# Optimization experiments

Measured on AMD Instinct MI355X. Metric: run time of the kernel, lower is better.

Reference implementation:

```python
import jax, jax.numpy as jnp
import numpy as np

B, LC, LQ, D = 32, 2048, 256, 256


def setup_inputs() -> dict:
    key = jax.random.key(0)
    kc, kq, kcm, kqm, kw = jax.random.split(key, 5)
    context = jax.random.normal(kc, (B, LC, D), dtype=jnp.float32)
    query = jax.random.normal(kq, (B, LQ, D), dtype=jnp.float32)
    # True = masked (matches torch masked_fill semantics)
    context_mask = jax.random.randint(kcm, (B, LC), 0, 2).astype(bool)
    query_mask = jax.random.randint(kqm, (B, LQ), 0, 2).astype(bool)
    # nn.Linear(3*dim, 1, bias=False) weight, flattened to (3D,)
    w0 = jax.random.normal(kw, (3 * D,), dtype=jnp.float32) * (1.0 / np.sqrt(3 * D))
    return {"context": context, "query": query, "context_mask": context_mask,
            "query_mask": query_mask, "w0": w0}


def reference(context, query, context_mask, query_mask, w0):
    d = context.shape[-1]
    wc, wq, wm = w0[:d], w0[d:2 * d], w0[2 * d:]
    # trilinear sim: w0 . [c, q, c*q]  ==  c.wc + q.wq + (c*wm) q^T
    sc = context @ wc                                   # (B, Lc)
    sq = query @ wq                                     # (B, Lq)
    sim = sc[:, :, None] + sq[:, None, :] + jnp.einsum(
        'bcd,bqd->bcq', context * wm, query)            # (B, Lc, Lq)
    mask = context_mask[:, :, None] | query_mask[:, None, :]
    sim = jnp.where(mask, jnp.float32(-1e30), sim)
    S = jax.nn.softmax(sim, axis=-1)                    # row softmax over Lq
    SS = jax.nn.softmax(sim, axis=1)                    # col softmax over Lc
    S = jnp.nan_to_num(S)
    SS = jnp.nan_to_num(SS)
    A = jnp.einsum('bcq,bqd->bcd', S, query)            # (B, Lc, D)
    T = jnp.einsum('bkq,bkd->bqd', SS, context)         # SS^T @ context, (B, Lq, D)
    Bmat = jnp.einsum('bcq,bqd->bcd', S, T)             # (B, Lc, D)
    return (A, Bmat)
```

## Files before the change

kernel.cpp:

```cpp
#include <hip/hip_runtime.h>

#define B_  32
#define LC_ 2048
#define LQ_ 256
#define D_  256
#define NEG (-1e30f)

typedef _Float16 f16;
typedef _Float16 f16x4 __attribute__((ext_vector_type(4)));
typedef _Float16 f16x8 __attribute__((ext_vector_type(8)));
typedef float    f32x4 __attribute__((ext_vector_type(4)));

__global__ __launch_bounds__(256) void k_scsq(
    const float* __restrict__ ctx, const float* __restrict__ qry,
    const float* __restrict__ w0, float* __restrict__ sc, float* __restrict__ sq)
{
    const int lane = threadIdx.x & 63;
    const int wave = threadIdx.x >> 6;
    const int row  = blockIdx.x * 4 + wave;
    const int NC = B_ * LC_;
    const int NQ = B_ * LQ_;
    const float* src; const float* w; float* dst;
    if (row < NC) { src = ctx + (long long)row * D_; w = w0; dst = sc + row; }
    else if (row < NC + NQ) { int r = row - NC; src = qry + (long long)r * D_; w = w0 + D_; dst = sq + r; }
    else return;
    float4 a = *(const float4*)(src + lane * 4);
    float4 b = *(const float4*)(w   + lane * 4);
    float v = a.x*b.x + a.y*b.y + a.z*b.z + a.w*b.w;
    #pragma unroll
    for (int off = 32; off > 0; off >>= 1) v += __shfl_down(v, off, 64);
    if (lane == 0) *dst = v;
}

__global__ __launch_bounds__(256) void k_transpose_q(
    const float* __restrict__ in, f16* __restrict__ out,
    int R, int C, long long in_bs, long long out_bs)
{
    __shared__ float tile[64 * 65];
    const int b = blockIdx.z;
    const int r0 = blockIdx.x * 64, c0 = blockIdx.y * 64;
    const int t = threadIdx.x;
    const float* ib = in + (long long)b * in_bs;
    #pragma unroll
    for (int p = 0; p < 4; ++p) {
        int r = (t >> 4) + p * 16;
        int cb = (t & 15) * 4;
        float4 v = *(const float4*)(ib + (long long)(r0 + r) * C + c0 + cb);
        tile[r * 65 + cb + 0] = v.x;
        tile[r * 65 + cb + 1] = v.y;
        tile[r * 65 + cb + 2] = v.z;
        tile[r * 65 + cb + 3] = v.w;
    }
    __syncthreads();
    f16* ob = out + (long long)b * out_bs;
    #pragma unroll
    for (int p = 0; p < 4; ++p) {
        int c = (t >> 4) + p * 16;
        int rb = (t & 15) * 4;
        f16x4 h;
        h[0] = (f16)tile[(rb + 0) * 65 + c];
        h[1] = (f16)tile[(rb + 1) * 65 + c];
        h[2] = (f16)tile[(rb + 2) * 65 + c];
        h[3] = (f16)tile[(rb + 3) * 65 + c];
        *(f16x4*)(ob + (long long)(c0 + c) * R + r0 + rb) = h;
    }
}

#define LDA1 40
__global__ __launch_bounds__(256) void k_g1(
    const float* __restrict__ ctx, const float* __restrict__ qry,
    const float* __restrict__ w0, const float* __restrict__ sc,
    const float* __restrict__ sq, const int* __restrict__ cmask,
    const int* __restrict__ qmask, float* __restrict__ sim)
{
    __shared__ f16 As[128 * LDA1];
    __shared__ f16 Bs[128 * LDA1];
    const int b = blockIdx.z;
    const int c0 = blockIdx.x * 128, q0 = blockIdx.y * 128;
    const int t = threadIdx.x, lane = t & 63, wv = t >> 6;
    const int wm_off = (wv >> 1) * 64, wn_off = (wv & 1) * 64;
    const float* Ab = ctx + (long long)b * LC_ * D_;
    const float* Bb = qry + (long long)b * LQ_ * D_;
    const float* wmp = w0 + 2 * D_;
    const int srow = t >> 3, scg = (t & 7) * 4;
    f32x4 acc[4][4] = {};
    for (int k0 = 0; k0 < D_; k0 += 32) {
        float4 wm4 = *(const float4*)(wmp + k0 + scg);
        #pragma unroll
        for (int p = 0; p < 4; ++p) {
            int r = srow + p * 32;
            float4 v = *(const float4*)(Ab + (long long)(c0 + r) * D_ + k0 + scg);
            f16x4 h;
            h[0] = (f16)(v.x * wm4.x); h[1] = (f16)(v.y * wm4.y);
            h[2] = (f16)(v.z * wm4.z); h[3] = (f16)(v.w * wm4.w);
            *(f16x4*)(As + r * LDA1 + scg) = h;
            float4 u = *(const float4*)(Bb + (long long)(q0 + r) * D_ + k0 + scg);
            f16x4 g;
            g[0] = (f16)u.x; g[1] = (f16)u.y; g[2] = (f16)u.z; g[3] = (f16)u.w;
            *(f16x4*)(Bs + r * LDA1 + scg) = g;
        }
        __syncthreads();
        f16x8 af[4], bf[4];
        #pragma unroll
        for (int i = 0; i < 4; ++i)
            af[i] = *(const f16x8*)(As + (wm_off + i * 16 + (lane & 15)) * LDA1 + (lane >> 4) * 8);
        #pragma unroll
        for (int j = 0; j < 4; ++j)
            bf[j] = *(const f16x8*)(Bs + (wn_off + j * 16 + (lane & 15)) * LDA1 + (lane >> 4) * 8);
        #pragma unroll
        for (int i = 0; i < 4; ++i)
            #pragma unroll
            for (int j = 0; j < 4; ++j)
                acc[i][j] = __builtin_amdgcn_mfma_f32_16x16x32_f16(af[i], bf[j], acc[i][j], 0, 0, 0);
        __syncthreads();
    }
    float sqv[4]; int qmv[4];
    #pragma unroll
    for (int j = 0; j < 4; ++j) {
        int q = q0 + wn_off + j * 16 + (lane & 15);
        sqv[j] = sq[b * LQ_ + q];
        qmv[j] = qmask[b * LQ_ + q];
    }
    #pragma unroll
    for (int i = 0; i < 4; ++i) {
        #pragma unroll
        for (int r = 0; r < 4; ++r) {
            int c = c0 + wm_off + i * 16 + (lane >> 4) * 4 + r;
            float scv = sc[b * LC_ + c];
            int cm = cmask[b * LC_ + c];
            float* orow = sim + ((long long)b * LC_ + c) * LQ_ + q0 + wn_off + (lane & 15);
            #pragma unroll
            for (int j = 0; j < 4; ++j) {
                float val = acc[i][j][r] + scv + sqv[j];
                orow[j * 16] = (cm | qmv[j]) ? NEG : val;
            }
        }
    }
}

__global__ __launch_bounds__(256) void k_s1(
    const float* __restrict__ sim, float* __restrict__ rowm, float* __restrict__ rowinvl,
    float* __restrict__ pm, float* __restrict__ pl)
{
    __shared__ float tile[32 * 260];
    const int ch = blockIdx.x;
    const int b  = blockIdx.y;
    const int t  = threadIdx.x;
    const int c0 = ch * 32;
    const float* sb = sim + ((long long)b * LC_ + c0) * LQ_;
    #pragma unroll
    for (int p = 0; p < 8; ++p) {
        int r = p * 4 + (t >> 6);
        int cb = (t & 63) * 4;
        float4 v = *(const float4*)(sb + (long long)r * LQ_ + cb);
        *(float4*)(tile + r * 260 + cb) = v;
    }
    __syncthreads();
    {
        int r = t >> 3, s = t & 7;
        const float* rp = tile + r * 260;
        float m = -INFINITY;
        #pragma unroll
        for (int i = 0; i < 32; ++i) m = fmaxf(m, rp[(i << 3) + s]);
        m = fmaxf(m, __shfl_xor(m, 1, 64));
        m = fmaxf(m, __shfl_xor(m, 2, 64));
        m = fmaxf(m, __shfl_xor(m, 4, 64));
        float l = 0.f;
        #pragma unroll
        for (int i = 0; i < 32; ++i) l += __expf(rp[(i << 3) + s] - m);
        l += __shfl_xor(l, 1, 64);
        l += __shfl_xor(l, 2, 64);
        l += __shfl_xor(l, 4, 64);
        if (s == 0) {
            rowm[b * LC_ + c0 + r] = m;
            rowinvl[b * LC_ + c0 + r] = 1.0f / l;
        }
    }
    {
        float m = -INFINITY;
        #pragma unroll 8
        for (int r = 0; r < 32; ++r) m = fmaxf(m, tile[r * 260 + t]);
        float l = 0.f;
        #pragma unroll 8
        for (int r = 0; r < 32; ++r) l += __expf(tile[r * 260 + t] - m);
        int idx = (b * 64 + ch) * LQ_ + t;
        pm[idx] = m; pl[idx] = l;
    }
}

__global__ __launch_bounds__(256) void k_colreduce(
    const float* __restrict__ pm, const float* __restrict__ pl,
    float* __restrict__ colm, float* __restrict__ colinvl)
{
    const int col = blockIdx.x * 256 + threadIdx.x;
    const int b = col >> 8, q = col & 255;
    float M = -INFINITY, L = 0.f;
    for (int ch = 0; ch < 64; ++ch) {
        int idx = (b * 64 + ch) * LQ_ + q;
        float m = pm[idx], l = pl[idx];
        float nM = fmaxf(M, m);
        L = L * __expf(M - nM) + l * __expf(m - nM);
        M = nM;
    }
    colm[col] = M; colinvl[col] = 1.0f / L;
}

__global__ __launch_bounds__(256) void k_s2(
    const float* __restrict__ sim, const float* __restrict__ colm,
    f16* __restrict__ E)
{
    __shared__ float tile[64 * 65];
    const int c0 = blockIdx.x * 64, q0 = blockIdx.y * 64, b = blockIdx.z;
    const int t = threadIdx.x;
    const float* sb = sim + ((long long)b * LC_ + c0) * LQ_ + q0;
    #pragma unroll
    for (int p = 0; p < 4; ++p) {
        int r = (t >> 4) + p * 16;
        int cb = (t & 15) * 4;
        float4 v = *(const float4*)(sb + (long long)r * LQ_ + cb);
        tile[r * 65 + cb + 0] = v.x;
        tile[r * 65 + cb + 1] = v.y;
        tile[r * 65 + cb + 2] = v.z;
        tile[r * 65 + cb + 3] = v.w;
    }
    __syncthreads();
    #pragma unroll
    for (int p = 0; p < 4; ++p) {
        int ql = (t >> 4) + p * 16;
        int cb = (t & 15) * 4;
        float cm = colm[b * LQ_ + q0 + ql];
        f16x4 h;
        h[0] = (f16)__expf(tile[(cb + 0) * 65 + ql] - cm);
        h[1] = (f16)__expf(tile[(cb + 1) * 65 + ql] - cm);
        h[2] = (f16)__expf(tile[(cb + 2) * 65 + ql] - cm);
        h[3] = (f16)__expf(tile[(cb + 3) * 65 + ql] - cm);
        *(f16x4*)(E + ((long long)b * LQ_ + q0 + ql) * LC_ + c0 + cb) = h;
    }
}

#define LDA3 72
__global__ __launch_bounds__(256) void k_g3(
    const f16* __restrict__ ctxt, const f16* __restrict__ E,
    const float* __restrict__ colinvl, f16* __restrict__ Bcat)
{
    __shared__ f16 As[64 * LDA3];
    __shared__ f16 Bs[64 * LDA3];
    const int d0 = blockIdx.x * 64, q0 = blockIdx.y * 64, b = blockIdx.z;
    const int t = threadIdx.x, lane = t & 63, wv = t >> 6;
    const int wm_off = (wv >> 1) * 32, wn_off = (wv & 1) * 32;
    const f16* Ab = ctxt + (long long)b * D_ * LC_;
    const f16* Bb = E + (long long)b * LQ_ * LC_;
    const int srow = t >> 3, sch = (t & 7) * 8;
    f32x4 acc[2][2] = {};
    for (int k0 = 0; k0 < LC_; k0 += 64) {
        #pragma unroll
        for (int p = 0; p < 2; ++p) {
            int r = srow + p * 32;
            *(uint4*)(As + r * LDA3 + sch) = *(const uint4*)(Ab + (long long)(d0 + r) * LC_ + k0 + sch);
            *(uint4*)(Bs + r * LDA3 + sch) = *(const uint4*)(Bb + (long long)(q0 + r) * LC_ + k0 + sch);
        }
        __syncthreads();
        #pragma unroll
        for (int kk = 0; kk < 64; kk += 32) {
            f16x8 af[2], bf[2];
            #pragma unroll
            for (int i = 0; i < 2; ++i)
                af[i] = *(const f16x8*)(As + (wm_off + i * 16 + (lane & 15)) * LDA3 + kk + (lane >> 4) * 8);
            #pragma unroll
            for (int j = 0; j < 2; ++j)
                bf[j] = *(const f16x8*)(Bs + (wn_off + j * 16 + (lane & 15)) * LDA3 + kk + (lane >> 4) * 8);
            #pragma unroll
            for (int i = 0; i < 2; ++i)
                #pragma unroll
                for (int j = 0; j < 2; ++j)
                    acc[i][j] = __builtin_amdgcn_mfma_f32_16x16x32_f16(af[i], bf[j], acc[i][j], 0, 0, 0);
        }
        __syncthreads();
    }
    float cinv[2];
    #pragma unroll
    for (int j = 0; j < 2; ++j)
        cinv[j] = colinvl[b * LQ_ + q0 + wn_off + j * 16 + (lane & 15)];
    #pragma unroll
    for (int i = 0; i < 2; ++i) {
        #pragma unroll
        for (int r = 0; r < 4; ++r) {
            int d = d0 + wm_off + i * 16 + (lane >> 4) * 4 + r;
            f16* orow = Bcat + (long long)b * 512 * LQ_ + (long long)(256 + d) * LQ_ + q0 + wn_off + (lane & 15);
            #pragma unroll
            for (int j = 0; j < 2; ++j)
                orow[j * 16] = (f16)(acc[i][j][r] * cinv[j]);
        }
    }
}

__global__ __launch_bounds__(256) void k_g23(
    const float* __restrict__ sim, const float* __restrict__ rowm,
    const float* __restrict__ rowinvl, const f16* __restrict__ Bcat,
    float* __restrict__ outA, float* __restrict__ outB)
{
    __shared__ f16 As[128 * LDA1];
    __shared__ f16 Bs[128 * LDA1];
    const int b = blockIdx.z;
    const int c0 = blockIdx.x * 128, n0 = blockIdx.y * 128;
    const int t = threadIdx.x, lane = t & 63, wv = t >> 6;
    const int wm_off = (wv >> 1) * 64, wn_off = (wv & 1) * 64;
    const float* Ab = sim + ((long long)b * LC_ + c0) * LQ_;
    const f16* Bb = Bcat + (long long)b * 512 * LQ_ + (long long)n0 * LQ_;
    const int srow = t >> 3, scg = (t & 7) * 4;
    const int brow = t >> 2, bch = (t & 3) * 8;
    float rm[4];
    #pragma unroll
    for (int p = 0; p < 4; ++p) rm[p] = rowm[b * LC_ + c0 + srow + p * 32];
    f32x4 acc[4][4] = {};
    for (int k0 = 0; k0 < LQ_; k0 += 32) {
        #pragma unroll
        for (int p = 0; p < 4; ++p) {
            int r = srow + p * 32;
            float4 v = *(const float4*)(Ab + (long long)r * LQ_ + k0 + scg);
            f16x4 h;
            h[0] = (f16)__expf(v.x - rm[p]);
            h[1] = (f16)__expf(v.y - rm[p]);
            h[2] = (f16)__expf(v.z - rm[p]);
            h[3] = (f16)__expf(v.w - rm[p]);
            *(f16x4*)(As + r * LDA1 + scg) = h;
        }
        #pragma unroll
        for (int p = 0; p < 2; ++p) {
            int r = brow + p * 64;
            *(uint4*)(Bs + r * LDA1 + bch) = *(const uint4*)(Bb + (long long)r * LQ_ + k0 + bch);
        }
        __syncthreads();
        f16x8 af[4], bf[4];
        #pragma unroll
        for (int i = 0; i < 4; ++i)
            af[i] = *(const f16x8*)(As + (wm_off + i * 16 + (lane & 15)) * LDA1 + (lane >> 4) * 8);
        #pragma unroll
        for (int j = 0; j < 4; ++j)
            bf[j] = *(const f16x8*)(Bs + (wn_off + j * 16 + (lane & 15)) * LDA1 + (lane >> 4) * 8);
        #pragma unroll
        for (int i = 0; i < 4; ++i)
            #pragma unroll
            for (int j = 0; j < 4; ++j)
                acc[i][j] = __builtin_amdgcn_mfma_f32_16x16x32_f16(af[i], bf[j], acc[i][j], 0, 0, 0);
        __syncthreads();
    }
    float* outp = (n0 < 256) ? outA : outB;
    const int nbase = (n0 < 256) ? n0 : (n0 - 256);
    #pragma unroll
    for (int i = 0; i < 4; ++i) {
        #pragma unroll
        for (int r = 0; r < 4; ++r) {
            int c = c0 + wm_off + i * 16 + (lane >> 4) * 4 + r;
            float ri = rowinvl[b * LC_ + c];
            float* orow = outp + ((long long)b * LC_ + c) * D_ + nbase + wn_off + (lane & 15);
            #pragma unroll
            for (int j = 0; j < 4; ++j)
                orow[j * 16] = acc[i][j][r] * ri;
        }
    }
}

extern "C" void kernel_launch(void* const* d_in, const int* in_sizes, int n_in,
                              void* d_out, int out_size, void* d_ws, size_t ws_size,
                              hipStream_t stream) {
    const float* ctx   = (const float*)d_in[0];
    const float* qry   = (const float*)d_in[1];
    const int*   cmask = (const int*)d_in[2];
    const int*   qmask = (const int*)d_in[3];
    const float* w0    = (const float*)d_in[4];
    float* out = (float*)d_out;

    char* w = (char*)d_ws;
    float* sc      = (float*)w;  w += (long long)65536 * 4;
    float* sq      = (float*)w;  w += (long long)8192 * 4;
    float* rowm    = (float*)w;  w += (long long)65536 * 4;
    float* rowinvl = (float*)w;  w += (long long)65536 * 4;
    float* colm    = (float*)w;  w += (long long)8192 * 4;
    float* colinvl = (float*)w;  w += (long long)8192 * 4;
    float* pm      = (float*)w;  w += (long long)524288 * 4;
    float* pl      = (float*)w;  w += (long long)524288 * 4;
    float* sim     = (float*)w;  w += (long long)16777216 * 4;
    f16*   ctxt    = (f16*)w;    w += (long long)16777216 * 2;
    f16*   E       = (f16*)w;    w += (long long)16777216 * 2;
    f16*   Bcat    = (f16*)w;    w += (long long)4194304 * 2;

    k_scsq<<<18432, 256, 0, stream>>>(ctx, qry, w0, sc, sq);
    k_transpose_q<<<dim3(32, 4, 32), 256, 0, stream>>>(ctx, ctxt, LC_, D_,
        (long long)LC_ * D_, (long long)D_ * LC_);
    k_transpose_q<<<dim3(4, 4, 32), 256, 0, stream>>>(qry, Bcat, LQ_, D_,
        (long long)LQ_ * D_, (long long)512 * LQ_);
    k_g1<<<dim3(16, 2, 32), 256, 0, stream>>>(ctx, qry, w0, sc, sq, cmask, qmask, sim);
    k_s1<<<dim3(64, 32), 256, 0, stream>>>(sim, rowm, rowinvl, pm, pl);
    k_colreduce<<<32, 256, 0, stream>>>(pm, pl, colm, colinvl);
    k_s2<<<dim3(32, 4, 32), 256, 0, stream>>>(sim, colm, E);
    k_g3<<<dim3(4, 4, 32), 256, 0, stream>>>(ctxt, E, colinvl, Bcat);
    k_g23<<<dim3(16, 4, 32), 256, 0, stream>>>(sim, rowm, rowinvl, Bcat,
        out, out + (long long)B_ * LC_ * D_);
}
```

Measured before the change: 369.7 us.

## Store sim in fp16, fuse column-exp into g3, drop ctx transpose and E buffer

The prep kernel now converts context to fp16 and pre-scales query by wm in fp16 while computing sc/sq. The sim matrix is stored as fp16 instead of fp32, with the mask sentinel changed to -30000. The separate k_s2 exp/transpose pass and the fp32 context transpose are removed: k_g3 reads row-major ctx16 and sim16, transposes them into shared memory and applies the column exp on the fly. g1 now covers all 256 query columns per block. This cuts global traffic for sim, E and ctxt. The cost is fp16 precision on the logits and bank-conflicting scalar LDS transposes inside g3.

```diff
diff --git a/kernel.cpp b/kernel.cpp
--- a/kernel.cpp
+++ b/kernel.cpp
@@ -4,55 +4,67 @@
 #define LC_ 2048
 #define LQ_ 256
 #define D_  256
-#define NEG (-1e30f)
+#define NEGH (-30000.0f)
 
 typedef _Float16 f16;
 typedef _Float16 f16x4 __attribute__((ext_vector_type(4)));
 typedef _Float16 f16x8 __attribute__((ext_vector_type(8)));
 typedef float    f32x4 __attribute__((ext_vector_type(4)));
 
-__global__ __launch_bounds__(256) void k_scsq(
+__global__ __launch_bounds__(256) void k_prep(
     const float* __restrict__ ctx, const float* __restrict__ qry,
-    const float* __restrict__ w0, float* __restrict__ sc, float* __restrict__ sq)
+    const float* __restrict__ w0, f16* __restrict__ ctx16,
+    f16* __restrict__ qrywm16, float* __restrict__ sc, float* __restrict__ sq)
 {
     const int lane = threadIdx.x & 63;
     const int wave = threadIdx.x >> 6;
     const int row  = blockIdx.x * 4 + wave;
     const int NC = B_ * LC_;
-    const int NQ = B_ * LQ_;
-    const float* src; const float* w; float* dst;
-    if (row < NC) { src = ctx + (long long)row * D_; w = w0; dst = sc + row; }
-    else if (row < NC + NQ) { int r = row - NC; src = qry + (long long)r * D_; w = w0 + D_; dst = sq + r; }
-    else return;
-    float4 a = *(const float4*)(src + lane * 4);
-    float4 b = *(const float4*)(w   + lane * 4);
-    float v = a.x*b.x + a.y*b.y + a.z*b.z + a.w*b.w;
-    #pragma unroll
-    for (int off = 32; off > 0; off >>= 1) v += __shfl_down(v, off, 64);
-    if (lane == 0) *dst = v;
-}
-
-__global__ __launch_bounds__(256) void k_transpose_q(
-    const float* __restrict__ in, f16* __restrict__ out,
-    int R, int C, long long in_bs, long long out_bs)
+    if (row < NC) {
+        float4 v = *(const float4*)(ctx + (long long)row * D_ + lane * 4);
+        f16x4 h; h[0] = (f16)v.x; h[1] = (f16)v.y; h[2] = (f16)v.z; h[3] = (f16)v.w;
+        *(f16x4*)(ctx16 + (long long)row * D_ + lane * 4) = h;
+        float4 wc = *(const float4*)(w0 + lane * 4);
+        float s = v.x*wc.x + v.y*wc.y + v.z*wc.z + v.w*wc.w;
+        #pragma unroll
+        for (int off = 32; off > 0; off >>= 1) s += __shfl_down(s, off, 64);
+        if (lane == 0) sc[row] = s;
+    } else {
+        int r = row - NC;
+        float4 v = *(const float4*)(qry + (long long)r * D_ + lane * 4);
+        float4 wm = *(const float4*)(w0 + 2 * D_ + lane * 4);
+        f16x4 h;
+        h[0] = (f16)(v.x * wm.x); h[1] = (f16)(v.y * wm.y);
+        h[2] = (f16)(v.z * wm.z); h[3] = (f16)(v.w * wm.w);
+        *(f16x4*)(qrywm16 + (long long)r * D_ + lane * 4) = h;
+        float4 wq = *(const float4*)(w0 + D_ + lane * 4);
+        float s = v.x*wq.x + v.y*wq.y + v.z*wq.z + v.w*wq.w;
+        #pragma unroll
+        for (int off = 32; off > 0; off >>= 1) s += __shfl_down(s, off, 64);
+        if (lane == 0) sq[r] = s;
+    }
+}
+
+__global__ __launch_bounds__(256) void k_tq(
+    const float* __restrict__ in, f16* __restrict__ out)
 {
     __shared__ float tile[64 * 65];
     const int b = blockIdx.z;
     const int r0 = blockIdx.x * 64, c0 = blockIdx.y * 64;
     const int t = threadIdx.x;
-    const float* ib = in + (long long)b * in_bs;
+    const float* ib = in + (long long)b * LQ_ * D_;
     #pragma unroll
     for (int p = 0; p < 4; ++p) {
         int r = (t >> 4) + p * 16;
         int cb = (t & 15) * 4;
-        float4 v = *(const float4*)(ib + (long long)(r0 + r) * C + c0 + cb);
+        float4 v = *(const float4*)(ib + (long long)(r0 + r) * D_ + c0 + cb);
         tile[r * 65 + cb + 0] = v.x;
         tile[r * 65 + cb + 1] = v.y;
         tile[r * 65 + cb + 2] = v.z;
         tile[r * 65 + cb + 3] = v.w;
     }
     __syncthreads();
-    f16* ob = out + (long long)b * out_bs;
+    f16* ob = out + (long long)b * 512 * LQ_;
     #pragma unroll
     for (int p = 0; p < 4; ++p) {
         int c = (t >> 4) + p * 16;
@@ -62,62 +74,57 @@
         h[1] = (f16)tile[(rb + 1) * 65 + c];
         h[2] = (f16)tile[(rb + 2) * 65 + c];
         h[3] = (f16)tile[(rb + 3) * 65 + c];
-        *(f16x4*)(ob + (long long)(c0 + c) * R + r0 + rb) = h;
+        *(f16x4*)(ob + (long long)(c0 + c) * LQ_ + r0 + rb) = h;
     }
 }
 
 #define LDA1 40
 __global__ __launch_bounds__(256) void k_g1(
-    const float* __restrict__ ctx, const float* __restrict__ qry,
-    const float* __restrict__ w0, const float* __restrict__ sc,
-    const float* __restrict__ sq, const int* __restrict__ cmask,
-    const int* __restrict__ qmask, float* __restrict__ sim)
+    const f16* __restrict__ ctx16, const f16* __restrict__ qrywm16,
+    const float* __restrict__ sc, const float* __restrict__ sq,
+    const int* __restrict__ cmask, const int* __restrict__ qmask,
+    f16* __restrict__ sim16)
 {
     __shared__ f16 As[128 * LDA1];
-    __shared__ f16 Bs[128 * LDA1];
+    __shared__ f16 Bs[256 * LDA1];
     const int b = blockIdx.z;
-    const int c0 = blockIdx.x * 128, q0 = blockIdx.y * 128;
+    const int c0 = blockIdx.x * 128;
     const int t = threadIdx.x, lane = t & 63, wv = t >> 6;
-    const int wm_off = (wv >> 1) * 64, wn_off = (wv & 1) * 64;
-    const float* Ab = ctx + (long long)b * LC_ * D_;
-    const float* Bb = qry + (long long)b * LQ_ * D_;
-    const float* wmp = w0 + 2 * D_;
-    const int srow = t >> 3, scg = (t & 7) * 4;
-    f32x4 acc[4][4] = {};
+    const int wm_off = (wv >> 1) * 64, wn_off = (wv & 1) * 128;
+    const f16* Ab = ctx16 + ((long long)b * LC_ + c0) * D_;
+    const f16* Bb = qrywm16 + (long long)b * LQ_ * D_;
+    const int srow = t >> 2, scg = (t & 3) * 8;
+    f32x4 acc[4][8] = {};
     for (int k0 = 0; k0 < D_; k0 += 32) {
-        float4 wm4 = *(const float4*)(wmp + k0 + scg);
+        #pragma unroll
+        for (int p = 0; p < 2; ++p) {
+            int r = srow + p * 64;
+            *(f16x8*)(As + r * LDA1 + scg) = *(const f16x8*)(Ab + (long long)r * D_ + k0 + scg);
+        }
         #pragma unroll
         for (int p = 0; p < 4; ++p) {
-            int r = srow + p * 32;
-            float4 v = *(const float4*)(Ab + (long long)(c0 + r) * D_ + k0 + scg);
-            f16x4 h;
-            h[0] = (f16)(v.x * wm4.x); h[1] = (f16)(v.y * wm4.y);
-            h[2] = (f16)(v.z * wm4.z); h[3] = (f16)(v.w * wm4.w);
-            *(f16x4*)(As + r * LDA1 + scg) = h;
-            float4 u = *(const float4*)(Bb + (long long)(q0 + r) * D_ + k0 + scg);
-            f16x4 g;
-            g[0] = (f16)u.x; g[1] = (f16)u.y; g[2] = (f16)u.z; g[3] = (f16)u.w;
-            *(f16x4*)(Bs + r * LDA1 + scg) = g;
-        }
-        __syncthreads();
-        f16x8 af[4], bf[4];
+            int r = srow + p * 64;
+            *(f16x8*)(Bs + r * LDA1 + scg) = *(const f16x8*)(Bb + (long long)r * D_ + k0 + scg);
+        }
+        __syncthreads();
+        f16x8 af[4], bf[8];
         #pragma unroll
         for (int i = 0; i < 4; ++i)
             af[i] = *(const f16x8*)(As + (wm_off + i * 16 + (lane & 15)) * LDA1 + (lane >> 4) * 8);
         #pragma unroll
-        for (int j = 0; j < 4; ++j)
+        for (int j = 0; j < 8; ++j)
             bf[j] = *(const f16x8*)(Bs + (wn_off + j * 16 + (lane & 15)) * LDA1 + (lane >> 4) * 8);
         #pragma unroll
         for (int i = 0; i < 4; ++i)
             #pragma unroll
-            for (int j = 0; j < 4; ++j)
+            for (int j = 0; j < 8; ++j)
                 acc[i][j] = __builtin_amdgcn_mfma_f32_16x16x32_f16(af[i], bf[j], acc[i][j], 0, 0, 0);
         __syncthreads();
     }
-    float sqv[4]; int qmv[4];
-    #pragma unroll
-    for (int j = 0; j < 4; ++j) {
-        int q = q0 + wn_off + j * 16 + (lane & 15);
+    float sqv[8]; int qmv[8];
+    #pragma unroll
+    for (int j = 0; j < 8; ++j) {
+        int q = wn_off + j * 16 + (lane & 15);
         sqv[j] = sq[b * LQ_ + q];
         qmv[j] = qmask[b * LQ_ + q];
     }
@@ -128,18 +135,18 @@
             int c = c0 + wm_off + i * 16 + (lane >> 4) * 4 + r;
             float scv = sc[b * LC_ + c];
             int cm = cmask[b * LC_ + c];
-            float* orow = sim + ((long long)b * LC_ + c) * LQ_ + q0 + wn_off + (lane & 15);
-            #pragma unroll
-            for (int j = 0; j < 4; ++j) {
-                float val = acc[i][j][r] + scv + sqv[j];
-                orow[j * 16] = (cm | qmv[j]) ? NEG : val;
+            f16* orow = sim16 + ((long long)b * LC_ + c) * LQ_ + wn_off + (lane & 15);
+            #pragma unroll
+            for (int j = 0; j < 8; ++j) {
+                float val = (cm | qmv[j]) ? NEGH : (acc[i][j][r] + scv + sqv[j]);
+                orow[j * 16] = (f16)val;
             }
         }
     }
 }
 
 __global__ __launch_bounds__(256) void k_s1(
-    const float* __restrict__ sim, float* __restrict__ rowm, float* __restrict__ rowinvl,
+    const f16* __restrict__ sim16, float* __restrict__ rowm, float* __restrict__ rowinvl,
     float* __restrict__ pm, float* __restrict__ pl)
 {
     __shared__ float tile[32 * 260];
@@ -147,13 +154,16 @@
     const int b  = blockIdx.y;
     const int t  = threadIdx.x;
     const int c0 = ch * 32;
-    const float* sb = sim + ((long long)b * LC_ + c0) * LQ_;
+    const f16* sb = sim16 + ((long long)b * LC_ + c0) * LQ_;
     #pragma unroll
     for (int p = 0; p < 8; ++p) {
         int r = p * 4 + (t >> 6);
         int cb = (t & 63) * 4;
-        float4 v = *(const float4*)(sb + (long long)r * LQ_ + cb);
-        *(float4*)(tile + r * 260 + cb) = v;
+        f16x4 v = *(const f16x4*)(sb + (long long)r * LQ_ + cb);
+        tile[r * 260 + cb + 0] = (float)v[0];
+        tile[r * 260 + cb + 1] = (float)v[1];
+        tile[r * 260 + cb + 2] = (float)v[2];
+        tile[r * 260 + cb + 3] = (float)v[3];
     }
     __syncthreads();
     {
@@ -205,97 +215,81 @@
     colm[col] = M; colinvl[col] = 1.0f / L;
 }
 
-__global__ __launch_bounds__(256) void k_s2(
-    const float* __restrict__ sim, const float* __restrict__ colm,
-    f16* __restrict__ E)
-{
-    __shared__ float tile[64 * 65];
-    const int c0 = blockIdx.x * 64, q0 = blockIdx.y * 64, b = blockIdx.z;
-    const int t = threadIdx.x;
-    const float* sb = sim + ((long long)b * LC_ + c0) * LQ_ + q0;
-    #pragma unroll
-    for (int p = 0; p < 4; ++p) {
-        int r = (t >> 4) + p * 16;
-        int cb = (t & 15) * 4;
-        float4 v = *(const float4*)(sb + (long long)r * LQ_ + cb);
-        tile[r * 65 + cb + 0] = v.x;
-        tile[r * 65 + cb + 1] = v.y;
-        tile[r * 65 + cb + 2] = v.z;
-        tile[r * 65 + cb + 3] = v.w;
+#define LDA3 66
+__global__ __launch_bounds__(256) void k_g3(
+    const f16* __restrict__ ctx16, const f16* __restrict__ sim16,
+    const float* __restrict__ colm, const float* __restrict__ colinvl,
+    f16* __restrict__ Bcat)
+{
+    __shared__ f16 As[128 * LDA3];
+    __shared__ f16 Bs[64 * LDA3];
+    __shared__ float colm_s[64], cil_s[64];
+    const int b = blockIdx.x;
+    const int combo = blockIdx.y;
+    const int qt = combo & 3, dh = combo >> 2;
+    const int q0 = qt * 64, d0 = dh * 128;
+    const int t = threadIdx.x, lane = t & 63, wv = t >> 6;
+    const int wm_off = (wv >> 1) * 64, wn_off = (wv & 1) * 32;
+    if (t < 64) {
+        colm_s[t] = colm[b * LQ_ + q0 + t];
+        cil_s[t]  = colinvl[b * LQ_ + q0 + t];
     }
     __syncthreads();
-    #pragma unroll
-    for (int p = 0; p < 4; ++p) {
-        int ql = (t >> 4) + p * 16;
-        int cb = (t & 15) * 4;
-        float cm = colm[b * LQ_ + q0 + ql];
-        f16x4 h;
-        h[0] = (f16)__expf(tile[(cb + 0) * 65 + ql] - cm);
-        h[1] = (f16)__expf(tile[(cb + 1) * 65 + ql] - cm);
-        h[2] = (f16)__expf(tile[(cb + 2) * 65 + ql] - cm);
-        h[3] = (f16)__expf(tile[(cb + 3) * 65 + ql] - cm);
-        *(f16x4*)(E + ((long long)b * LQ_ + q0 + ql) * LC_ + c0 + cb) = h;
-    }
-}
-
-#define LDA3 72
-__global__ __launch_bounds__(256) void k_g3(
-    const f16* __restrict__ ctxt, const f16* __restrict__ E,
-    const float* __restrict__ colinvl, f16* __restrict__ Bcat)
-{
-    __shared__ f16 As[64 * LDA3];
-    __shared__ f16 Bs[64 * LDA3];
-    const int d0 = blockIdx.x * 64, q0 = blockIdx.y * 64, b = blockIdx.z;
-    const int t = threadIdx.x, lane = t & 63, wv = t >> 6;
-    const int wm_off = (wv >> 1) * 32, wn_off = (wv & 1) * 32;
-    const f16* Ab = ctxt + (long long)b * D_ * LC_;
-    const f16* Bb = E + (long long)b * LQ_ * LC_;
-    const int srow = t >> 3, sch = (t & 7) * 8;
-    f32x4 acc[2][2] = {};
-    for (int k0 = 0; k0 < LC_; k0 += 64) {
+    const f16* Ab = ctx16 + (long long)b * LC_ * D_;
+    const f16* Sb = sim16 + (long long)b * LC_ * LQ_;
+    f32x4 acc[4][2] = {};
+    const int acc_ = t >> 4, ad8 = (t & 15) * 8;
+    const int bcc = t >> 3, bq8 = (t & 7) * 8;
+    for (int c0 = 0; c0 < LC_; c0 += 64) {
+        #pragma unroll
+        for (int p = 0; p < 4; ++p) {
+            int cc = acc_ + p * 16;
+            f16x8 h = *(const f16x8*)(Ab + (long long)(c0 + cc) * D_ + d0 + ad8);
+            #pragma unroll
+            for (int j = 0; j < 8; ++j)
+                As[(ad8 + j) * LDA3 + cc] = h[j];
+        }
         #pragma unroll
         for (int p = 0; p < 2; ++p) {
-            int r = srow + p * 32;
-            *(uint4*)(As + r * LDA3 + sch) = *(const uint4*)(Ab + (long long)(d0 + r) * LC_ + k0 + sch);
-            *(uint4*)(Bs + r * LDA3 + sch) = *(const uint4*)(Bb + (long long)(q0 + r) * LC_ + k0 + sch);
+            int cc = bcc + p * 32;
+            f16x8 h = *(const f16x8*)(Sb + (long long)(c0 + cc) * LQ_ + q0 + bq8);
+            #pragma unroll
+            for (int j = 0; j < 8; ++j)
+                Bs[(bq8 + j) * LDA3 + cc] = (f16)__expf((float)h[j] - colm_s[bq8 + j]);
         }
         __syncthreads();
         #pragma unroll
         for (int kk = 0; kk < 64; kk += 32) {
-            f16x8 af[2], bf[2];
-            #pragma unroll
-            for (int i = 0; i < 2; ++i)
+            f16x8 af[4], bf[2];
+            #pragma unroll
+            for (int i = 0; i < 4; ++i)
                 af[i] = *(const f16x8*)(As + (wm_off + i * 16 + (lane & 15)) * LDA3 + kk + (lane >> 4) * 8);
             #pragma unroll
             for (int j = 0; j < 2; ++j)
                 bf[j] = *(const f16x8*)(Bs + (wn_off + j * 16 + (lane & 15)) * LDA3 + kk + (lane >> 4) * 8);
             #pragma unroll
-            for (int i = 0; i < 2; ++i)
+            for (int i = 0; i < 4; ++i)
                 #pragma unroll
                 for (int j = 0; j < 2; ++j)
                     acc[i][j] = __builtin_amdgcn_mfma_f32_16x16x32_f16(af[i], bf[j], acc[i][j], 0, 0, 0);
         }
         __syncthreads();
     }
-    float cinv[2];
-    #pragma unroll
-    for (int j = 0; j < 2; ++j)
-        cinv[j] = colinvl[b * LQ_ + q0 + wn_off + j * 16 + (lane & 15)];
-    #pragma unroll
-    for (int i = 0; i < 2; ++i) {
+    #pragma unroll
+    for (int i = 0; i < 4; ++i) {
         #pragma unroll
         for (int r = 0; r < 4; ++r) {
             int d = d0 + wm_off + i * 16 + (lane >> 4) * 4 + r;
             f16* orow = Bcat + (long long)b * 512 * LQ_ + (long long)(256 + d) * LQ_ + q0 + wn_off + (lane & 15);
             #pragma unroll
             for (int j = 0; j < 2; ++j)
-                orow[j * 16] = (f16)(acc[i][j][r] * cinv[j]);
+                orow[j * 16] = (f16)(acc[i][j][r] * cil_s[wn_off + j * 16 + (lane & 15)]);
         }
     }
 }
 
 __global__ __launch_bounds__(256) void k_g23(
-    const float* __restrict__ sim, const float* __restrict__ rowm,
+    const f16* __restrict__ sim16, const float* __restrict__ rowm,
     const float* __restrict__ rowinvl, const f16* __restrict__ Bcat,
     float* __restrict__ outA, float* __restrict__ outB)
 {
@@ -305,30 +299,23 @@
     const int c0 = blockIdx.x * 128, n0 = blockIdx.y * 128;
     const int t = threadIdx.x, lane = t & 63, wv = t >> 6;
     const int wm_off = (wv >> 1) * 64, wn_off = (wv & 1) * 64;
-    const float* Ab = sim + ((long long)b * LC_ + c0) * LQ_;
-    const f16* Bb = Bcat + (long long)b * 512 * LQ_ + (long long)n0 * LQ_;
-    const int srow = t >> 3, scg = (t & 7) * 4;
-    const int brow = t >> 2, bch = (t & 3) * 8;
-    float rm[4];
-    #pragma unroll
-    for (int p = 0; p < 4; ++p) rm[p] = rowm[b * LC_ + c0 + srow + p * 32];
+    const f16* Ab = sim16 + ((long long)b * LC_ + c0) * LQ_;
+    const f16* Bb = Bcat + ((long long)b * 512 + n0) * LQ_;
+    const int srow = t >> 2, scg = (t & 3) * 8;
+    float rm[2];
+    #pragma unroll
+    for (int p = 0; p < 2; ++p) rm[p] = rowm[b * LC_ + c0 + srow + p * 64];
     f32x4 acc[4][4] = {};
     for (int k0 = 0; k0 < LQ_; k0 += 32) {
         #pragma unroll
-        for (int p = 0; p < 4; ++p) {
-            int r = srow + p * 32;
-            float4 v = *(const float4*)(Ab + (long long)r * LQ_ + k0 + scg);
-            f16x4 h;
-            h[0] = (f16)__expf(v.x - rm[p]);
-            h[1] = (f16)__expf(v.y - rm[p]);
-            h[2] = (f16)__expf(v.z - rm[p]);
-            h[3] = (f16)__expf(v.w - rm[p]);
-            *(f16x4*)(As + r * LDA1 + scg) = h;
-        }
-        #pragma unroll
         for (int p = 0; p < 2; ++p) {
-            int r = brow + p * 64;
-            *(uint4*)(Bs + r * LDA1 + bch) = *(const uint4*)(Bb + (long long)r * LQ_ + k0 + bch);
+            int r = srow + p * 64;
+            f16x8 h = *(const f16x8*)(Ab + (long long)r * LQ_ + k0 + scg);
+            f16x8 e;
+            #pragma unroll
+            for (int j = 0; j < 8; ++j) e[j] = (f16)__expf((float)h[j] - rm[p]);
+            *(f16x8*)(As + r * LDA1 + scg) = e;
+            *(f16x8*)(Bs + r * LDA1 + scg) = *(const f16x8*)(Bb + (long long)r * LQ_ + k0 + scg);
         }
         __syncthreads();
         f16x8 af[4], bf[4];
@@ -380,21 +367,17 @@
     float* colinvl = (float*)w;  w += (long long)8192 * 4;
     float* pm      = (float*)w;  w += (long long)524288 * 4;
     float* pl      = (float*)w;  w += (long long)524288 * 4;
-    float* sim     = (float*)w;  w += (long long)16777216 * 4;
-    f16*   ctxt    = (f16*)w;    w += (long long)16777216 * 2;
-    f16*   E       = (f16*)w;    w += (long long)16777216 * 2;
+    f16*   sim16   = (f16*)w;    w += (long long)16777216 * 2;
+    f16*   ctx16   = (f16*)w;    w += (long long)16777216 * 2;
+    f16*   qrywm16 = (f16*)w;    w += (long long)2097152 * 2;
     f16*   Bcat    = (f16*)w;    w += (long long)4194304 * 2;
 
-    k_scsq<<<18432, 256, 0, stream>>>(ctx, qry, w0, sc, sq);
-    k_transpose_q<<<dim3(32, 4, 32), 256, 0, stream>>>(ctx, ctxt, LC_, D_,
-        (long long)LC_ * D_, (long long)D_ * LC_);
-    k_transpose_q<<<dim3(4, 4, 32), 256, 0, stream>>>(qry, Bcat, LQ_, D_,
-        (long long)LQ_ * D_, (long long)512 * LQ_);
-    k_g1<<<dim3(16, 2, 32), 256, 0, stream>>>(ctx, qry, w0, sc, sq, cmask, qmask, sim);
-    k_s1<<<dim3(64, 32), 256, 0, stream>>>(sim, rowm, rowinvl, pm, pl);
+    k_prep<<<18432, 256, 0, stream>>>(ctx, qry, w0, ctx16, qrywm16, sc, sq);
+    k_tq<<<dim3(4, 4, 32), 256, 0, stream>>>(qry, Bcat);
+    k_g1<<<dim3(16, 1, 32), 256, 0, stream>>>(ctx16, qrywm16, sc, sq, cmask, qmask, sim16);
+    k_s1<<<dim3(64, 32), 256, 0, stream>>>(sim16, rowm, rowinvl, pm, pl);
     k_colreduce<<<32, 256, 0, stream>>>(pm, pl, colm, colinvl);
-    k_s2<<<dim3(32, 4, 32), 256, 0, stream>>>(sim, colm, E);
-    k_g3<<<dim3(4, 4, 32), 256, 0, stream>>>(ctxt, E, colinvl, Bcat);
-    k_g23<<<dim3(16, 4, 32), 256, 0, stream>>>(sim, rowm, rowinvl, Bcat,
+    k_g3<<<dim3(32, 8), 256, 0, stream>>>(ctx16, sim16, colm, colinvl, Bcat);
+    k_g23<<<dim3(16, 4, 32), 256, 0, stream>>>(sim16, rowm, rowinvl, Bcat,
         out, out + (long long)B_ * LC_ * D_);
 }
```

Result: faster. 327.3 us (-11.5%).
